# Kernel tuning notes

Hardware: AMD Instinct MI355X
Metric: run time of the kernel (lower is better)

## Reference

```python
import jax, jax.numpy as jnp
import numpy as np

B, H, N, D = 2, 16, 2048, 128

def setup_inputs() -> dict:
    key = jax.random.key(0)
    kq, kk, kv = jax.random.split(key, 3)
    q = jax.random.normal(kq, (B, H, N, D), dtype=jnp.float32)
    k = jax.random.normal(kk, (B, H, N, D), dtype=jnp.float32)
    v = jax.random.normal(kv, (B, H, N, D), dtype=jnp.float32)
    return {"q": q, "k": k, "v": v}

def reference(q, k, v):
    # scale = 1/sqrt(d) computed at forward time (scale=None in __init__)
    d = q.shape[-1]
    scale = 1.0 / jnp.sqrt(jnp.asarray(d, dtype=q.dtype))
    # scores: (B, H, N, N)
    scores = jnp.einsum('bhnd,bhmd->bhnm', q, k) * scale
    probs = jax.nn.softmax(scores, axis=-1)
    return jnp.einsum('bhnm,bhmd->bhnd', probs, v)
```

## Files before the change

### kernel.cpp

```cpp
#include <hip/hip_runtime.h>
#include <hip/hip_fp16.h>

#define BH   32
#define SEQ  2048
#define DIM  128
#define CK   32
#define NCH  (SEQ / CK)

typedef _Float16 half8   __attribute__((ext_vector_type(8)));
typedef __fp16   fp16x2  __attribute__((ext_vector_type(2)));
typedef _Float16 half2v  __attribute__((ext_vector_type(2)));
typedef float    floatx4 __attribute__((ext_vector_type(4)));

__device__ inline half2v pk2(float a, float b) {
    fp16x2 t = __builtin_amdgcn_cvt_pkrtz(a, b);
    return *(half2v*)&t;
}
__device__ inline half8 pk8(float4 a, float4 b) {
    half2v l0 = pk2(a.x, a.y), l1 = pk2(a.z, a.w);
    half2v l2 = pk2(b.x, b.y), l3 = pk2(b.z, b.w);
    half8 h;
    h[0] = l0[0]; h[1] = l0[1]; h[2] = l1[0]; h[3] = l1[1];
    h[4] = l2[0]; h[5] = l2[1]; h[6] = l3[0]; h[7] = l3[1];
    return h;
}

__device__ inline void ld16(const void* g, void* l) {
    __builtin_amdgcn_global_load_lds(
        (__attribute__((address_space(1))) void*)(uintptr_t)g,
        (__attribute__((address_space(3))) void*)(uintptr_t)l, 16, 0, 0);
}

#define SYNC_VM0 do {                                          \
    asm volatile("s_waitcnt vmcnt(0)" ::: "memory");           \
    __builtin_amdgcn_s_barrier();                              \
    asm volatile("" ::: "memory");                             \
} while (0)

__global__ void prep_kernel(const float* __restrict__ k, const float* __restrict__ v,
                            _Float16* __restrict__ kh, _Float16* __restrict__ vt) {
    const float SC = 0.08838834764831845f * 1.4426950408889634f;
    __shared__ __align__(16) _Float16 t[32][136];
    const int bh = blockIdx.x >> 6;
    const int kc = blockIdx.x & 63;
    const int tid = threadIdx.x;
    const size_t base = ((size_t)bh * SEQ + kc * CK) * DIM;

    const float4* kf4 = (const float4*)(k + base);
    const float4* vf4 = (const float4*)(v + base);
    half8* kh8 = (half8*)(kh + base);

    #pragma unroll
    for (int i = 0; i < 2; i++) {
        int f8 = i * 256 + tid;
        float4 a = kf4[2 * f8], b = kf4[2 * f8 + 1];
        a.x *= SC; a.y *= SC; a.z *= SC; a.w *= SC;
        b.x *= SC; b.y *= SC; b.z *= SC; b.w *= SC;
        kh8[f8] = pk8(a, b);
        int row = f8 >> 4, c8 = f8 & 15;
        *((half8*)&t[row][c8 * 8]) = pk8(vf4[2 * f8], vf4[2 * f8 + 1]);
    }
    __syncthreads();
    _Float16* vout = vt + ((size_t)bh * NCH + kc) * (DIM * CK);
    #pragma unroll
    for (int i = 0; i < 2; i++) {
        int g = i * 256 + tid;
        int d = g >> 2, kg = g & 3;
        half8 h;
        #pragma unroll
        for (int j = 0; j < 8; j++) h[j] = t[kg * 8 + j][d];
        *((half8*)(vout + d * CK + kg * 8)) = h;
    }
}

__global__ __launch_bounds__(256, 2) void attn_kernel(
        const float* __restrict__ q, const _Float16* __restrict__ kh,
        const _Float16* __restrict__ vt, float* __restrict__ out) {
    __shared__ __align__(16) _Float16 Kbuf[2][CK * DIM];
    __shared__ __align__(16) _Float16 Vbuf[3][DIM * CK];

    const int lid = blockIdx.x + (blockIdx.y << 4);
    const int xcd = lid & 7;
    const int idx = lid >> 3;
    const int bh  = (xcd << 2) + (idx >> 4);
    const int qt  = idx & 15;

    const int tid  = threadIdx.x;
    const int w    = tid >> 6;
    const int lane = tid & 63;
    const int l15  = lane & 15;
    const int quad = lane >> 4;

    {
        float4 z4 = {0.f, 0.f, 0.f, 0.f};
        ((float4*)&Vbuf[2][0])[tid] = z4;
        ((float4*)&Vbuf[2][0])[tid + 256] = z4;
        asm volatile("s_waitcnt lgkmcnt(0)" ::: "memory");
    }

    half8 qf[2][4];
    #pragma unroll
    for (int s = 0; s < 2; s++) {
        const float* qb = q + ((size_t)bh * SEQ + qt * 128 + w * 32 + s * 16 + l15) * DIM;
        #pragma unroll
        for (int c = 0; c < 4; c++) {
            float4 a = *((const float4*)(qb + c * 32 + quad * 8));
            float4 b = *((const float4*)(qb + c * 32 + quad * 8 + 4));
            qf[s][c] = pk8(a, b);
        }
    }

    half8 ones;
    #pragma unroll
    for (int j = 0; j < 8; j++) ones[j] = (_Float16)1.0f;

    floatx4 zf = {0.f, 0.f, 0.f, 0.f};
    floatx4 O[2][8];
    #pragma unroll
    for (int s = 0; s < 2; s++)
        #pragma unroll
        for (int i = 0; i < 8; i++) O[s][i] = zf;
    floatx4 Osum[2] = {zf, zf};

    const _Float16* kb = kh + (size_t)bh * SEQ * DIM;
    const _Float16* vb = vt + (size_t)bh * SEQ * DIM;

    const int s0 = w * 128 + lane;
    const int s1 = s0 + 64;
    const int rho0 = s0 >> 4, Pos0 = s0 & 15;
    const int rho1 = s1 >> 4, Pos1 = s1 & 15;
    const int g0 = (Pos0 - 3 * rho0) & 15;
    const int g1 = (Pos1 - 3 * rho1) & 15;
    const int key0 = (((rho0 >> 2) & 3) << 3) + ((rho0 >> 4) << 2) + (rho0 & 3);
    const int key1 = (((rho1 >> 2) & 3) << 3) + ((rho1 >> 4) << 2) + (rho1 & 3);
    const _Float16* kgp0 = kb + key0 * DIM + g0 * 8;
    const _Float16* kgp1 = kb + key1 * DIM + g1 * 8;
    const int vo0 = ((s0 >> 6) * 16 + (s0 & 15)) * CK + ((s0 >> 4) & 3) * 8;
    const int vo1 = ((s1 >> 6) * 16 + (s1 & 15)) * CK + ((s1 >> 4) & 3) * 8;
    const _Float16* vgp0 = vb + vo0;
    const _Float16* vgp1 = vb + vo1;

    auto dma = [&](int kc, int bk_, int bv_) {
        size_t off = (size_t)kc * (CK * DIM);
        ld16(kgp0 + off, &Kbuf[bk_][(w * 2 + 0) * 512]);
        ld16(kgp1 + off, &Kbuf[bk_][(w * 2 + 1) * 512]);
        ld16(vgp0 + off, &Vbuf[bv_][(w * 2 + 0) * 512]);
        ld16(vgp1 + off, &Vbuf[bv_][(w * 2 + 1) * 512]);
    };

    half8 pf0, pf1;
    #pragma unroll
    for (int j = 0; j < 8; j++) { pf0[j] = (_Float16)0.0f; pf1[j] = (_Float16)0.0f; }

    auto body = [&](int bk_, int bvp_) {
        const _Float16* Kc = Kbuf[bk_];

        floatx4 S[2][2];
        #pragma unroll
        for (int s = 0; s < 2; s++) { S[s][0] = zf; S[s][1] = zf; }
        __builtin_amdgcn_s_setprio(1);
        #pragma unroll
        for (int c = 0; c < 4; c++) {
            #pragma unroll
            for (int j = 0; j < 2; j++) {
                int rho = j * 16 + l15;
                int Pos = (c * 4 + quad + 3 * rho) & 15;
                half8 ka = *((const half8*)&Kc[rho * DIM + Pos * 8]);
                S[0][j] = __builtin_amdgcn_mfma_f32_16x16x32_f16(ka, qf[0][c], S[0][j], 0, 0, 0);
                S[1][j] = __builtin_amdgcn_mfma_f32_16x16x32_f16(ka, qf[1][c], S[1][j], 0, 0, 0);
            }
        }
        __builtin_amdgcn_s_setprio(0);

        const _Float16* Vp = Vbuf[bvp_];
        half8 vfr[8];
        #pragma unroll
        for (int dt = 0; dt < 8; dt++)
            vfr[dt] = *((const half8*)&Vp[dt * 512 + (quad * 16 + l15) * 8]);

        half8 pn0, pn1;
        {
            float4 a, b;
            a.x = __builtin_amdgcn_exp2f(S[0][0][0]);
            a.y = __builtin_amdgcn_exp2f(S[0][0][1]);
            a.z = __builtin_amdgcn_exp2f(S[0][0][2]);
            a.w = __builtin_amdgcn_exp2f(S[0][0][3]);
            b.x = __builtin_amdgcn_exp2f(S[0][1][0]);
            b.y = __builtin_amdgcn_exp2f(S[0][1][1]);
            b.z = __builtin_amdgcn_exp2f(S[0][1][2]);
            b.w = __builtin_amdgcn_exp2f(S[0][1][3]);
            pn0 = pk8(a, b);
            a.x = __builtin_amdgcn_exp2f(S[1][0][0]);
            a.y = __builtin_amdgcn_exp2f(S[1][0][1]);
            a.z = __builtin_amdgcn_exp2f(S[1][0][2]);
            a.w = __builtin_amdgcn_exp2f(S[1][0][3]);
            b.x = __builtin_amdgcn_exp2f(S[1][1][0]);
            b.y = __builtin_amdgcn_exp2f(S[1][1][1]);
            b.z = __builtin_amdgcn_exp2f(S[1][1][2]);
            b.w = __builtin_amdgcn_exp2f(S[1][1][3]);
            pn1 = pk8(a, b);
        }

        __builtin_amdgcn_s_setprio(1);
        Osum[0] = __builtin_amdgcn_mfma_f32_16x16x32_f16(pf0, ones, Osum[0], 0, 0, 0);
        Osum[1] = __builtin_amdgcn_mfma_f32_16x16x32_f16(pf1, ones, Osum[1], 0, 0, 0);
        #pragma unroll
        for (int dt = 0; dt < 8; dt++) {
            O[0][dt] = __builtin_amdgcn_mfma_f32_16x16x32_f16(pf0, vfr[dt], O[0][dt], 0, 0, 0);
            O[1][dt] = __builtin_amdgcn_mfma_f32_16x16x32_f16(pf1, vfr[dt], O[1][dt], 0, 0, 0);
        }
        __builtin_amdgcn_s_setprio(0);

        pf0 = pn0; pf1 = pn1;
    };

    dma(0, 0, 0);

    int bvn = 1, bvp = 2;
    #pragma unroll 6
    for (int kc = 0; kc < NCH - 1; kc++) {
        SYNC_VM0;
        dma(kc + 1, (kc + 1) & 1, bvn);
        body(kc & 1, bvp);
        bvn++; if (bvn == 3) bvn = 0;
        bvp++; if (bvp == 3) bvp = 0;
    }

    SYNC_VM0;
    body((NCH - 1) & 1, bvp);

    {
        const _Float16* Vl = Vbuf[(NCH - 1) % 3];
        half8 vfl[8];
        #pragma unroll
        for (int dt = 0; dt < 8; dt++)
            vfl[dt] = *((const half8*)&Vl[dt * 512 + (quad * 16 + l15) * 8]);
        __builtin_amdgcn_s_setprio(1);
        Osum[0] = __builtin_amdgcn_mfma_f32_16x16x32_f16(pf0, ones, Osum[0], 0, 0, 0);
        Osum[1] = __builtin_amdgcn_mfma_f32_16x16x32_f16(pf1, ones, Osum[1], 0, 0, 0);
        #pragma unroll
        for (int dt = 0; dt < 8; dt++) {
            O[0][dt] = __builtin_amdgcn_mfma_f32_16x16x32_f16(pf0, vfl[dt], O[0][dt], 0, 0, 0);
            O[1][dt] = __builtin_amdgcn_mfma_f32_16x16x32_f16(pf1, vfl[dt], O[1][dt], 0, 0, 0);
        }
        __builtin_amdgcn_s_setprio(0);
    }

    #pragma unroll
    for (int s = 0; s < 2; s++) {
        float* ob = out + ((size_t)bh * SEQ + qt * 128 + w * 32 + s * 16) * DIM;
        #pragma unroll
        for (int r = 0; r < 4; r++) {
            float rinv = 1.0f / Osum[s][r];
            #pragma unroll
            for (int dt = 0; dt < 8; dt++) {
                ob[(size_t)(quad * 4 + r) * DIM + dt * 16 + l15] = O[s][dt][r] * rinv;
            }
        }
    }
}

extern "C" void kernel_launch(void* const* d_in, const int* in_sizes, int n_in,
                              void* d_out, int out_size, void* d_ws, size_t ws_size,
                              hipStream_t stream) {
    const float* q = (const float*)d_in[0];
    const float* k = (const float*)d_in[1];
    const float* v = (const float*)d_in[2];
    float* out = (float*)d_out;

    const size_t elems = (size_t)BH * SEQ * DIM;
    _Float16* kh = (_Float16*)d_ws;
    _Float16* vtp = kh + elems;

    prep_kernel<<<BH * NCH, 256, 0, stream>>>(k, v, kh, vtp);
    attn_kernel<<<dim3(SEQ / 128, BH), 256, 0, stream>>>(q, kh, vtp, out);
}
```

Before: 189.1 us.

## Load V fragments straight from global into registers, bypassing LDS

V tiles are no longer staged through a triple-buffered LDS ring. Each wave now loads its V fragments directly from global memory into registers at the end of each iteration, ready for the next iteration's P·V MFMAs. The barrier wait is relaxed to vmcnt(8), so only the K DMA must finish and the V register loads can stay in flight. This frees LDS and removes the LDS read step for V. The cost is that each of the four waves fetches the same V chunk from L2, and the global load latency is exposed to the register pipeline.

```diff
diff --git a/kernel.cpp b/kernel.cpp
--- a/kernel.cpp
+++ b/kernel.cpp
@@ -31,8 +31,8 @@
         (__attribute__((address_space(3))) void*)(uintptr_t)l, 16, 0, 0);
 }
 
-#define SYNC_VM0 do {                                          \
-    asm volatile("s_waitcnt vmcnt(0)" ::: "memory");           \
+#define SYNC_VM8 do {                                          \
+    asm volatile("s_waitcnt vmcnt(8)" ::: "memory");           \
     __builtin_amdgcn_s_barrier();                              \
     asm volatile("" ::: "memory");                             \
 } while (0)
@@ -77,7 +77,6 @@
         const float* __restrict__ q, const _Float16* __restrict__ kh,
         const _Float16* __restrict__ vt, float* __restrict__ out) {
     __shared__ __align__(16) _Float16 Kbuf[2][CK * DIM];
-    __shared__ __align__(16) _Float16 Vbuf[3][DIM * CK];
 
     const int lid = blockIdx.x + (blockIdx.y << 4);
     const int xcd = lid & 7;
@@ -90,13 +89,6 @@
     const int lane = tid & 63;
     const int l15  = lane & 15;
     const int quad = lane >> 4;
-
-    {
-        float4 z4 = {0.f, 0.f, 0.f, 0.f};
-        ((float4*)&Vbuf[2][0])[tid] = z4;
-        ((float4*)&Vbuf[2][0])[tid + 256] = z4;
-        asm volatile("s_waitcnt lgkmcnt(0)" ::: "memory");
-    }
 
     half8 qf[2][4];
     #pragma unroll
@@ -135,25 +127,35 @@
     const int key1 = (((rho1 >> 2) & 3) << 3) + ((rho1 >> 4) << 2) + (rho1 & 3);
     const _Float16* kgp0 = kb + key0 * DIM + g0 * 8;
     const _Float16* kgp1 = kb + key1 * DIM + g1 * 8;
-    const int vo0 = ((s0 >> 6) * 16 + (s0 & 15)) * CK + ((s0 >> 4) & 3) * 8;
-    const int vo1 = ((s1 >> 6) * 16 + (s1 & 15)) * CK + ((s1 >> 4) & 3) * 8;
-    const _Float16* vgp0 = vb + vo0;
-    const _Float16* vgp1 = vb + vo1;
-
-    auto dma = [&](int kc, int bk_, int bv_) {
+
+    auto dma = [&](int kc, int bk_) {
         size_t off = (size_t)kc * (CK * DIM);
         ld16(kgp0 + off, &Kbuf[bk_][(w * 2 + 0) * 512]);
         ld16(kgp1 + off, &Kbuf[bk_][(w * 2 + 1) * 512]);
-        ld16(vgp0 + off, &Vbuf[bv_][(w * 2 + 0) * 512]);
-        ld16(vgp1 + off, &Vbuf[bv_][(w * 2 + 1) * 512]);
     };
 
+    const _Float16* vlp = vb + l15 * CK + quad * 8;
+    half8 vfr[8];
+    auto vload = [&](int kc) {
+        const _Float16* p = vlp + (size_t)kc * (CK * DIM);
+        #pragma unroll
+        for (int dt = 0; dt < 8; dt++)
+            vfr[dt] = *((const half8*)(p + dt * 512));
+    };
+
     half8 pf0, pf1;
     #pragma unroll
     for (int j = 0; j < 8; j++) { pf0[j] = (_Float16)0.0f; pf1[j] = (_Float16)0.0f; }
 
-    auto body = [&](int bk_, int bvp_) {
-        const _Float16* Kc = Kbuf[bk_];
+    dma(0, 0);
+    vload(0);
+
+    #pragma unroll 2
+    for (int kc = 0; kc < NCH; kc++) {
+        SYNC_VM8;
+        if (kc + 1 < NCH) dma(kc + 1, (kc + 1) & 1);
+
+        const _Float16* Kc = Kbuf[kc & 1];
 
         floatx4 S[2][2];
         #pragma unroll
@@ -171,12 +173,6 @@
             }
         }
         __builtin_amdgcn_s_setprio(0);
-
-        const _Float16* Vp = Vbuf[bvp_];
-        half8 vfr[8];
-        #pragma unroll
-        for (int dt = 0; dt < 8; dt++)
-            vfr[dt] = *((const half8*)&Vp[dt * 512 + (quad * 16 + l15) * 8]);
 
         half8 pn0, pn1;
         {
@@ -211,37 +207,19 @@
         }
         __builtin_amdgcn_s_setprio(0);
 
+        vload(kc);
+
         pf0 = pn0; pf1 = pn1;
-    };
-
-    dma(0, 0, 0);
-
-    int bvn = 1, bvp = 2;
-    #pragma unroll 6
-    for (int kc = 0; kc < NCH - 1; kc++) {
-        SYNC_VM0;
-        dma(kc + 1, (kc + 1) & 1, bvn);
-        body(kc & 1, bvp);
-        bvn++; if (bvn == 3) bvn = 0;
-        bvp++; if (bvp == 3) bvp = 0;
-    }
-
-    SYNC_VM0;
-    body((NCH - 1) & 1, bvp);
+    }
 
     {
-        const _Float16* Vl = Vbuf[(NCH - 1) % 3];
-        half8 vfl[8];
-        #pragma unroll
-        for (int dt = 0; dt < 8; dt++)
-            vfl[dt] = *((const half8*)&Vl[dt * 512 + (quad * 16 + l15) * 8]);
         __builtin_amdgcn_s_setprio(1);
         Osum[0] = __builtin_amdgcn_mfma_f32_16x16x32_f16(pf0, ones, Osum[0], 0, 0, 0);
         Osum[1] = __builtin_amdgcn_mfma_f32_16x16x32_f16(pf1, ones, Osum[1], 0, 0, 0);
         #pragma unroll
         for (int dt = 0; dt < 8; dt++) {
-            O[0][dt] = __builtin_amdgcn_mfma_f32_16x16x32_f16(pf0, vfl[dt], O[0][dt], 0, 0, 0);
-            O[1][dt] = __builtin_amdgcn_mfma_f32_16x16x32_f16(pf1, vfl[dt], O[1][dt], 0, 0, 0);
+            O[0][dt] = __builtin_amdgcn_mfma_f32_16x16x32_f16(pf0, vfr[dt], O[0][dt], 0, 0, 0);
+            O[1][dt] = __builtin_amdgcn_mfma_f32_16x16x32_f16(pf1, vfr[dt], O[1][dt], 0, 0, 0);
         }
         __builtin_amdgcn_s_setprio(0);
     }
```

Result: slower. 207.5 us (+9.8%).

## Restructure software pipeline to interleave PV MFMAs with K fragment loads

Applied to the files above, without the earlier changes.

Restructures the main loop so the previous chunk's P·V MFMAs run first, interleaved with split LDS loads of K fragments, followed by the QK MFMAs. V fragments for the current chunk are then loaded into registers that persist across iterations. This removes the zeroed third V buffer and the separate final body, and lowers unroll from 6 to 2. The intent is to hide LDS latency behind MFMA work and cut code size. The cost is more live registers (vfr held across iterations) and a per-iteration branch on the prefetch.

```diff
diff --git a/kernel.cpp b/kernel.cpp
--- a/kernel.cpp
+++ b/kernel.cpp
@@ -90,13 +90,6 @@
     const int lane = tid & 63;
     const int l15  = lane & 15;
     const int quad = lane >> 4;
-
-    {
-        float4 z4 = {0.f, 0.f, 0.f, 0.f};
-        ((float4*)&Vbuf[2][0])[tid] = z4;
-        ((float4*)&Vbuf[2][0])[tid + 256] = z4;
-        asm volatile("s_waitcnt lgkmcnt(0)" ::: "memory");
-    }
 
     half8 qf[2][4];
     #pragma unroll
@@ -149,36 +142,83 @@
     };
 
     half8 pf0, pf1;
+    half8 vfr[8];
     #pragma unroll
     for (int j = 0; j < 8; j++) { pf0[j] = (_Float16)0.0f; pf1[j] = (_Float16)0.0f; }
-
-    auto body = [&](int bk_, int bvp_) {
-        const _Float16* Kc = Kbuf[bk_];
-
-        floatx4 S[2][2];
-        #pragma unroll
-        for (int s = 0; s < 2; s++) { S[s][0] = zf; S[s][1] = zf; }
-        __builtin_amdgcn_s_setprio(1);
-        #pragma unroll
-        for (int c = 0; c < 4; c++) {
+    #pragma unroll
+    for (int dt = 0; dt < 8; dt++)
+        #pragma unroll
+        for (int j = 0; j < 8; j++) vfr[dt][j] = (_Float16)0.0f;
+
+    dma(0, 0, 0);
+
+    int bvr = 0, bvn = 1;
+    #pragma unroll 2
+    for (int kc = 0; kc < NCH; kc++) {
+        SYNC_VM0;
+        if (kc + 1 < NCH) dma(kc + 1, (kc + 1) & 1, bvn);
+
+        const _Float16* Kc = Kbuf[kc & 1];
+        const _Float16* Vc = Vbuf[bvr];
+
+        half8 ka[4];
+        #pragma unroll
+        for (int c = 0; c < 2; c++)
             #pragma unroll
             for (int j = 0; j < 2; j++) {
                 int rho = j * 16 + l15;
                 int Pos = (c * 4 + quad + 3 * rho) & 15;
-                half8 ka = *((const half8*)&Kc[rho * DIM + Pos * 8]);
-                S[0][j] = __builtin_amdgcn_mfma_f32_16x16x32_f16(ka, qf[0][c], S[0][j], 0, 0, 0);
-                S[1][j] = __builtin_amdgcn_mfma_f32_16x16x32_f16(ka, qf[1][c], S[1][j], 0, 0, 0);
-            }
-        }
-        __builtin_amdgcn_s_setprio(0);
-
-        const _Float16* Vp = Vbuf[bvp_];
-        half8 vfr[8];
+                ka[c * 2 + j] = *((const half8*)&Kc[rho * DIM + Pos * 8]);
+            }
+
+        __builtin_amdgcn_s_setprio(1);
+        Osum[0] = __builtin_amdgcn_mfma_f32_16x16x32_f16(pf0, ones, Osum[0], 0, 0, 0);
         #pragma unroll
         for (int dt = 0; dt < 8; dt++)
-            vfr[dt] = *((const half8*)&Vp[dt * 512 + (quad * 16 + l15) * 8]);
-
-        half8 pn0, pn1;
+            O[0][dt] = __builtin_amdgcn_mfma_f32_16x16x32_f16(pf0, vfr[dt], O[0][dt], 0, 0, 0);
+        __builtin_amdgcn_s_setprio(0);
+
+        half8 kb2[4];
+        #pragma unroll
+        for (int c = 0; c < 2; c++)
+            #pragma unroll
+            for (int j = 0; j < 2; j++) {
+                int rho = j * 16 + l15;
+                int Pos = ((c + 2) * 4 + quad + 3 * rho) & 15;
+                kb2[c * 2 + j] = *((const half8*)&Kc[rho * DIM + Pos * 8]);
+            }
+
+        __builtin_amdgcn_s_setprio(1);
+        Osum[1] = __builtin_amdgcn_mfma_f32_16x16x32_f16(pf1, ones, Osum[1], 0, 0, 0);
+        #pragma unroll
+        for (int dt = 0; dt < 8; dt++)
+            O[1][dt] = __builtin_amdgcn_mfma_f32_16x16x32_f16(pf1, vfr[dt], O[1][dt], 0, 0, 0);
+        __builtin_amdgcn_s_setprio(0);
+
+        floatx4 S[2][2];
+        #pragma unroll
+        for (int s = 0; s < 2; s++) { S[s][0] = zf; S[s][1] = zf; }
+        __builtin_amdgcn_s_setprio(1);
+        #pragma unroll
+        for (int c = 0; c < 2; c++)
+            #pragma unroll
+            for (int j = 0; j < 2; j++) {
+                S[0][j] = __builtin_amdgcn_mfma_f32_16x16x32_f16(ka[c * 2 + j], qf[0][c], S[0][j], 0, 0, 0);
+                S[1][j] = __builtin_amdgcn_mfma_f32_16x16x32_f16(ka[c * 2 + j], qf[1][c], S[1][j], 0, 0, 0);
+            }
+        #pragma unroll
+        for (int c = 0; c < 2; c++)
+            #pragma unroll
+            for (int j = 0; j < 2; j++) {
+                S[0][j] = __builtin_amdgcn_mfma_f32_16x16x32_f16(kb2[c * 2 + j], qf[0][c + 2], S[0][j], 0, 0, 0);
+                S[1][j] = __builtin_amdgcn_mfma_f32_16x16x32_f16(kb2[c * 2 + j], qf[1][c + 2], S[1][j], 0, 0, 0);
+            }
+        __builtin_amdgcn_s_setprio(0);
+
+        #pragma unroll
+        for (int dt = 0; dt < 8; dt++)
+            vfr[dt] = *((const half8*)&Vc[dt * 512 + (quad * 16 + l15) * 8]);
+
         {
             float4 a, b;
             a.x = __builtin_amdgcn_exp2f(S[0][0][0]);
@@ -189,7 +229,7 @@
             b.y = __builtin_amdgcn_exp2f(S[0][1][1]);
             b.z = __builtin_amdgcn_exp2f(S[0][1][2]);
             b.w = __builtin_amdgcn_exp2f(S[0][1][3]);
-            pn0 = pk8(a, b);
+            pf0 = pk8(a, b);
             a.x = __builtin_amdgcn_exp2f(S[1][0][0]);
             a.y = __builtin_amdgcn_exp2f(S[1][0][1]);
             a.z = __builtin_amdgcn_exp2f(S[1][0][2]);
@@ -198,9 +238,14 @@
             b.y = __builtin_amdgcn_exp2f(S[1][1][1]);
             b.z = __builtin_amdgcn_exp2f(S[1][1][2]);
             b.w = __builtin_amdgcn_exp2f(S[1][1][3]);
-            pn1 = pk8(a, b);
-        }
-
+            pf1 = pk8(a, b);
+        }
+
+        bvr++; if (bvr == 3) bvr = 0;
+        bvn++; if (bvn == 3) bvn = 0;
+    }
+
+    {
         __builtin_amdgcn_s_setprio(1);
         Osum[0] = __builtin_amdgcn_mfma_f32_16x16x32_f16(pf0, ones, Osum[0], 0, 0, 0);
         Osum[1] = __builtin_amdgcn_mfma_f32_16x16x32_f16(pf1, ones, Osum[1], 0, 0, 0);
@@ -208,40 +253,6 @@
         for (int dt = 0; dt < 8; dt++) {
             O[0][dt] = __builtin_amdgcn_mfma_f32_16x16x32_f16(pf0, vfr[dt], O[0][dt], 0, 0, 0);
             O[1][dt] = __builtin_amdgcn_mfma_f32_16x16x32_f16(pf1, vfr[dt], O[1][dt], 0, 0, 0);
-        }
-        __builtin_amdgcn_s_setprio(0);
-
-        pf0 = pn0; pf1 = pn1;
-    };
-
-    dma(0, 0, 0);
-
-    int bvn = 1, bvp = 2;
-    #pragma unroll 6
-    for (int kc = 0; kc < NCH - 1; kc++) {
-        SYNC_VM0;
-        dma(kc + 1, (kc + 1) & 1, bvn);
-        body(kc & 1, bvp);
-        bvn++; if (bvn == 3) bvn = 0;
-        bvp++; if (bvp == 3) bvp = 0;
-    }
-
-    SYNC_VM0;
-    body((NCH - 1) & 1, bvp);
-
-    {
-        const _Float16* Vl = Vbuf[(NCH - 1) % 3];
-        half8 vfl[8];
-        #pragma unroll
-        for (int dt = 0; dt < 8; dt++)
-            vfl[dt] = *((const half8*)&Vl[dt * 512 + (quad * 16 + l15) * 8]);
-        __builtin_amdgcn_s_setprio(1);
-        Osum[0] = __builtin_amdgcn_mfma_f32_16x16x32_f16(pf0, ones, Osum[0], 0, 0, 0);
-        Osum[1] = __builtin_amdgcn_mfma_f32_16x16x32_f16(pf1, ones, Osum[1], 0, 0, 0);
-        #pragma unroll
-        for (int dt = 0; dt < 8; dt++) {
-            O[0][dt] = __builtin_amdgcn_mfma_f32_16x16x32_f16(pf0, vfl[dt], O[0][dt], 0, 0, 0);
-            O[1][dt] = __builtin_amdgcn_mfma_f32_16x16x32_f16(pf1, vfl[dt], O[1][dt], 0, 0, 0);
         }
         __builtin_amdgcn_s_setprio(0);
     }
```

Result: slower. 194.5 us (+2.9%).
